# Kernel tuning notes

Hardware: AMD Instinct MI355X
Metric: run time of the kernel (lower is better)

## Reference

```python
import jax, jax.numpy as jnp
import numpy as np

HEADS = 8
MODEL_DIM = 64
IN_DIM = 512
FF_DIM = 2048
LN_EPS = 1e-5


def _ln(t, g, b):
    m = t.mean(-1, keepdims=True)
    v = ((t - m) ** 2).mean(-1, keepdims=True)
    return (t - m) * jax.lax.rsqrt(v + LN_EPS) * g + b


def setup_inputs() -> dict:
    key = jax.random.key(0)
    ks = jax.random.split(key, 12)
    s = 1.0 / np.sqrt(IN_DIM)
    x = jax.random.normal(ks[0], (8, 32, 32, IN_DIM), dtype=jnp.float32)
    Wq = jax.random.uniform(ks[1], (IN_DIM, HEADS * MODEL_DIM), jnp.float32, -s, s)
    Wk = jax.random.uniform(ks[2], (IN_DIM, HEADS * MODEL_DIM), jnp.float32, -s, s)
    Wv = jax.random.uniform(ks[3], (IN_DIM, HEADS * MODEL_DIM), jnp.float32, -s, s)
    Wo = jax.random.uniform(ks[4], (HEADS * MODEL_DIM, IN_DIM), jnp.float32, -s, s)
    ln1_g = jnp.ones((IN_DIM,), jnp.float32)
    ln1_b = jnp.zeros((IN_DIM,), jnp.float32)
    fc1_w = jax.random.uniform(ks[5], (IN_DIM, FF_DIM), jnp.float32, -s, s)
    fc1_b = jnp.zeros((FF_DIM,), jnp.float32)
    s2 = 1.0 / np.sqrt(FF_DIM)
    fc2_w = jax.random.uniform(ks[6], (FF_DIM, IN_DIM), jnp.float32, -s2, s2)
    fc2_b = jnp.zeros((IN_DIM,), jnp.float32)
    ln2_g = jnp.ones((IN_DIM,), jnp.float32)
    ln2_b = jnp.zeros((IN_DIM,), jnp.float32)
    return {"x": x, "Wq": Wq, "Wk": Wk, "Wv": Wv, "Wo": Wo,
            "ln1_g": ln1_g, "ln1_b": ln1_b,
            "fc1_w": fc1_w, "fc1_b": fc1_b, "fc2_w": fc2_w, "fc2_b": fc2_b,
            "ln2_g": ln2_g, "ln2_b": ln2_b}


def reference(x, Wq, Wk, Wv, Wo, ln1_g, ln1_b, fc1_w, fc1_b, fc2_w, fc2_b, ln2_g, ln2_b):
    bs, h, w, c = x.shape
    # --- BertSelfAttention (pre_norm=True) ---
    xn = _ln(x, ln1_g, ln1_b)
    Q = (xn @ Wq).reshape(bs, h, w, HEADS, MODEL_DIM)
    K = (xn @ Wk).reshape(bs, h, w, HEADS, MODEL_DIM)
    V = (xn @ Wv).reshape(bs, h, w, HEADS, MODEL_DIM)
    scores = jnp.einsum('bijhd,bklhd->bijhkl', Q, K) / jnp.sqrt(jnp.float32(MODEL_DIM))
    probs = jax.nn.softmax(scores.reshape(bs, h, w, HEADS, h * w), axis=-1)
    probs = probs.reshape(bs, h, w, HEADS, h, w)
    o = jnp.einsum('bijhkl,bklhd->bijhd', probs, V).reshape(bs, h, w, HEADS * MODEL_DIM)
    attn_out = o @ Wo + xn  # residual adds pre-normed x (as in the torch code)
    # --- Feedforward (pre_norm=True) ---
    yn = _ln(attn_out, ln2_g, ln2_b)
    out = jax.nn.relu(yn @ fc1_w + fc1_b) @ fc2_w + fc2_b + yn
    return (out, probs)
```

## Files before the change

### kernel.cpp

```cpp
#include <hip/hip_runtime.h>

typedef unsigned short u16;
typedef unsigned int   u32;
typedef short s16x8 __attribute__((ext_vector_type(8)));
typedef float f32x4 __attribute__((ext_vector_type(4)));

#define EPI_QK  0
#define EPI_VT  1
#define EPI_RES 2
#define EPI_FC1 3
#define EPI_FC2 4

__device__ __forceinline__ u16 f2bf(float f) {
    u32 u = __float_as_uint(f);
    u32 r = u + 0x7FFFu + ((u >> 16) & 1u);
    return (u16)(r >> 16);
}
__device__ __forceinline__ s16x8 ld8(const u16* p) {
    return *(const s16x8*)p;
}
__device__ __forceinline__ void gload_lds16(const void* g, void* l) {
    __builtin_amdgcn_global_load_lds(
        (const __attribute__((address_space(1))) unsigned int*)g,
        (__attribute__((address_space(3))) unsigned int*)l, 16, 0, 0);
}


__device__ __forceinline__ void transpose_body(
    const float* __restrict__ W, u16* __restrict__ Wt, int Kd, int Nd,
    int bx, int by, float (*tls)[33])
{
    const int k0 = bx * 32, n0 = by * 32;
    const int r = threadIdx.x >> 3, c4 = (threadIdx.x & 7) * 4;
    float4 v = *(const float4*)&W[(size_t)(k0 + r) * Nd + n0 + c4];
    tls[r][c4] = v.x; tls[r][c4 + 1] = v.y; tls[r][c4 + 2] = v.z; tls[r][c4 + 3] = v.w;
    __syncthreads();
    u32 lo = (u32)f2bf(tls[c4][r])     | ((u32)f2bf(tls[c4 + 1][r]) << 16);
    u32 hi = (u32)f2bf(tls[c4 + 2][r]) | ((u32)f2bf(tls[c4 + 3][r]) << 16);
    uint2 pk; pk.x = lo; pk.y = hi;
    *(uint2*)&Wt[(size_t)(n0 + r) * Kd + k0 + c4] = pk;
}

__device__ __forceinline__ void ln_body(
    const float* __restrict__ x, const float* __restrict__ g, const float* __restrict__ bb,
    float* __restrict__ of, u16* __restrict__ ob, int tb)
{
    const int wave = threadIdx.x >> 6, lane = threadIdx.x & 63;
    const int t = tb * 4 + wave;
    const float* row = x + (size_t)t * 512;
    float4 v0 = *(const float4*)&row[lane * 8];
    float4 v1 = *(const float4*)&row[lane * 8 + 4];
    float s  = v0.x + v0.y + v0.z + v0.w + v1.x + v1.y + v1.z + v1.w;
    float sq = v0.x*v0.x + v0.y*v0.y + v0.z*v0.z + v0.w*v0.w
             + v1.x*v1.x + v1.y*v1.y + v1.z*v1.z + v1.w*v1.w;
#pragma unroll
    for (int o = 1; o < 64; o <<= 1) { s += __shfl_xor(s, o, 64); sq += __shfl_xor(sq, o, 64); }
    float mean = s * (1.f / 512.f);
    float var  = sq * (1.f / 512.f) - mean * mean;
    float rs = rsqrtf(var + 1e-5f);
    float4 g0 = *(const float4*)&g[lane * 8];
    float4 g1 = *(const float4*)&g[lane * 8 + 4];
    float4 b0 = *(const float4*)&bb[lane * 8];
    float4 b1 = *(const float4*)&bb[lane * 8 + 4];
    float y[8];
    y[0] = (v0.x - mean) * rs * g0.x + b0.x;
    y[1] = (v0.y - mean) * rs * g0.y + b0.y;
    y[2] = (v0.z - mean) * rs * g0.z + b0.z;
    y[3] = (v0.w - mean) * rs * g0.w + b0.w;
    y[4] = (v1.x - mean) * rs * g1.x + b1.x;
    y[5] = (v1.y - mean) * rs * g1.y + b1.y;
    y[6] = (v1.z - mean) * rs * g1.z + b1.z;
    y[7] = (v1.w - mean) * rs * g1.w + b1.w;
    float4 o0; o0.x = y[0]; o0.y = y[1]; o0.z = y[2]; o0.w = y[3];
    float4 o1; o1.x = y[4]; o1.y = y[5]; o1.z = y[6]; o1.w = y[7];
    *(float4*)&of[(size_t)t * 512 + lane * 8]     = o0;
    *(float4*)&of[(size_t)t * 512 + lane * 8 + 4] = o1;
    uint4 pb;
    pb.x = (u32)f2bf(y[0]) | ((u32)f2bf(y[1]) << 16);
    pb.y = (u32)f2bf(y[2]) | ((u32)f2bf(y[3]) << 16);
    pb.z = (u32)f2bf(y[4]) | ((u32)f2bf(y[5]) << 16);
    pb.w = (u32)f2bf(y[6]) | ((u32)f2bf(y[7]) << 16);
    *(uint4*)&ob[(size_t)t * 512 + lane * 8] = pb;
}

__device__ __forceinline__ void gemm_loop(
    const u16* __restrict__ A, const u16* __restrict__ Bt,
    int K, int m0, int n0, u16* sA, u16* sB, f32x4 (&acc)[4][4])
{
    const int tid = threadIdx.x;
    const int wave = tid >> 6, lane = tid & 63;
    const int wr = (wave >> 1) * 64, wc = (wave & 1) * 64;
    const int lr = lane & 15, quad = lane >> 4;

    const int p0 = wave * 64 + lane;
    const int r0 = p0 >> 2,          c0 = p0 & 3;
    const int r1 = (p0 + 256) >> 2;
    const u16* gA0 = A  + (size_t)(m0 + r0) * K + c0 * 8;
    const u16* gA1 = A  + (size_t)(m0 + r1) * K + c0 * 8;
    const u16* gB0 = Bt + (size_t)(n0 + r0) * K + c0 * 8;
    const u16* gB1 = Bt + (size_t)(n0 + r1) * K + c0 * 8;
    u16* lA0 = sA + (size_t)(wave * 64) * 8;
    u16* lA1 = sA + (size_t)(256 + wave * 64) * 8;
    u16* lB0 = sB + (size_t)(wave * 64) * 8;
    u16* lB1 = sB + (size_t)(256 + wave * 64) * 8;

    for (int k0 = 0; k0 < K; k0 += 32) {
        __syncthreads();
        gload_lds16(gA0 + k0, lA0);
        gload_lds16(gA1 + k0, lA1);
        gload_lds16(gB0 + k0, lB0);
        gload_lds16(gB1 + k0, lB1);
        __syncthreads();
        s16x8 a[4], b[4];
#pragma unroll
        for (int i = 0; i < 4; i++) a[i] = ld8(&sA[(wr + i * 16 + lr) * 32 + quad * 8]);
#pragma unroll
        for (int j = 0; j < 4; j++) b[j] = ld8(&sB[(wc + j * 16 + lr) * 32 + quad * 8]);
#pragma unroll
        for (int i = 0; i < 4; i++)
#pragma unroll
            for (int j = 0; j < 4; j++)
                acc[i][j] = __builtin_amdgcn_mfma_f32_16x16x32_bf16(a[i], b[j], acc[i][j], 0, 0, 0);
    }
}

__global__ __launch_bounds__(256) void prep_kernel(
    const float* __restrict__ Wq, const float* __restrict__ Wk,
    const float* __restrict__ Wv, const float* __restrict__ Wo,
    const float* __restrict__ fc1_w, const float* __restrict__ fc2_w,
    u16* __restrict__ WqT, u16* __restrict__ WkT, u16* __restrict__ WvT,
    u16* __restrict__ WoT, u16* __restrict__ fc1T, u16* __restrict__ fc2T,
    const float* __restrict__ x, const float* __restrict__ g,
    const float* __restrict__ bb, float* __restrict__ of, u16* __restrict__ ob)
{
    __shared__ float tls[32][33];
    const int id = blockIdx.x;
    if (id < 1024) {
        const int sel = id >> 8, r = id & 255;
        const float* W = (sel == 0) ? Wq : (sel == 1) ? Wk : (sel == 2) ? Wv : Wo;
        u16* Wt        = (sel == 0) ? WqT : (sel == 1) ? WkT : (sel == 2) ? WvT : WoT;
        transpose_body(W, Wt, 512, 512, r & 15, r >> 4, tls);
    } else if (id < 2048) {
        const int r = id - 1024;
        transpose_body(fc1_w, fc1T, 512, 2048, r & 15, r >> 4, tls);
    } else if (id < 3072) {
        const int r = id - 2048;
        transpose_body(fc2_w, fc2T, 2048, 512, r & 63, r >> 6, tls);
    } else {
        ln_body(x, g, bb, of, ob, id - 3072);
    }
}

__global__ __launch_bounds__(256) void ln_kernel(
    const float* __restrict__ x, const float* __restrict__ g, const float* __restrict__ bb,
    float* __restrict__ of, u16* __restrict__ ob)
{
    ln_body(x, g, bb, of, ob, blockIdx.x);
}

__global__ __launch_bounds__(256) void qkvt_gemm(
    const u16* __restrict__ xn_b, const u16* __restrict__ WqT, const u16* __restrict__ WvT,
    u16* __restrict__ Q_s, u16* __restrict__ K_s, u16* __restrict__ Vt_s)
{
    __shared__ u16 sA[128 * 32];
    __shared__ u16 sB[128 * 32];
    const int id = blockIdx.x;
    const u16 *A, *Bt;
    int m0, n0, epi;
    if (id < 512) { epi = EPI_QK; A = xn_b; Bt = WqT; n0 = (id & 7) * 128;  m0 = (id >> 3) * 128; }
    else { const int i2 = id - 512;
           epi = EPI_VT; A = WvT;  Bt = xn_b; n0 = (i2 & 63) * 128; m0 = (i2 >> 6) * 128; }

    f32x4 acc[4][4] = {};
    gemm_loop(A, Bt, 512, m0, n0, sA, sB, acc);

    const int lane = threadIdx.x & 63, wave = threadIdx.x >> 6;
    const int wr = (wave >> 1) * 64, wc = (wave & 1) * 64;
    const int lr = lane & 15, quad = lane >> 4;
#pragma unroll
    for (int i = 0; i < 4; i++)
#pragma unroll
    for (int j = 0; j < 4; j++)
#pragma unroll
    for (int r = 0; r < 4; r++) {
        int row = m0 + wr + i * 16 + quad * 4 + r;
        int col = n0 + wc + j * 16 + lr;
        float v = acc[i][j][r];
        if (epi == EPI_QK) {
            u16* dst = (col < 512) ? Q_s : K_s;
            int c2 = col & 511;
            size_t idx = (size_t)((row >> 10) * 8 + (c2 >> 6)) * 65536
                       + (size_t)(row & 1023) * 64 + (c2 & 63);
            dst[idx] = f2bf(v);
        } else {
            size_t idx = (size_t)((col >> 10) * 8 + (row >> 6)) * 65536
                       + (size_t)(row & 63) * 1024 + (col & 1023);
            Vt_s[idx] = f2bf(v);
        }
    }
}

template<int EPI>
__global__ __launch_bounds__(256) void gemm128(
    const u16* __restrict__ A, const u16* __restrict__ Bt,
    void* __restrict__ Out, void* __restrict__ Out2,
    const float* __restrict__ bias, const float* __restrict__ res,
    int M, int N, int K)
{
    __shared__ u16 sA[128 * 32];
    __shared__ u16 sB[128 * 32];
    const int n0 = blockIdx.x * 128, m0 = blockIdx.y * 128;

    f32x4 acc[4][4] = {};
    gemm_loop(A, Bt, K, m0, n0, sA, sB, acc);

    const int lane = threadIdx.x & 63, wave = threadIdx.x >> 6;
    const int wr = (wave >> 1) * 64, wc = (wave & 1) * 64;
    const int lr = lane & 15, quad = lane >> 4;
#pragma unroll
    for (int i = 0; i < 4; i++)
#pragma unroll
    for (int j = 0; j < 4; j++)
#pragma unroll
    for (int r = 0; r < 4; r++) {
        int row = m0 + wr + i * 16 + quad * 4 + r;
        int col = n0 + wc + j * 16 + lr;
        float v = acc[i][j][r];
        if (EPI == EPI_RES) {
            size_t idx = (size_t)row * N + col;
            ((float*)Out)[idx] = v + res[idx];
        } else if (EPI == EPI_FC1) {
            v += bias[col];
            v = fmaxf(v, 0.f);
            ((u16*)Out)[(size_t)row * N + col] = f2bf(v);
        } else {
            size_t idx = (size_t)row * N + col;
            ((float*)Out)[idx] = v + bias[col] + res[idx];
        }
    }
}

__global__ __launch_bounds__(256) void attn_kernel(
    const u16* __restrict__ Qs, const u16* __restrict__ Ks, const u16* __restrict__ Vts,
    float* __restrict__ probs, u16* __restrict__ Os)
{
    __shared__ u16 sK[2][64 * 72];
    __shared__ u16 sV[2][64 * 72];
    __shared__ u16 sP[4][16 * 72];
    const int bh = blockIdx.x;
    const int q0 = blockIdx.y * 64;
    const int b = bh >> 3, h = bh & 7;
    const int tid = threadIdx.x, wave = tid >> 6, lane = tid & 63;
    const int lr = lane & 15, quad = lane >> 4;
    const float scale = 0.125f;

    const u16* qb = Qs + (size_t)bh * 65536 + (size_t)(q0 + wave * 16 + lr) * 64 + quad * 8;
    const s16x8 bq0 = ld8(qb);
    const s16x8 bq1 = ld8(qb + 32);

    const int sr0 = tid >> 3, sr1 = sr0 + 32;
    const int sc  = (tid & 7) * 8;
    const u16* Kg = Ks  + (size_t)bh * 65536;
    const u16* Vg = Vts + (size_t)bh * 65536;

    {
        uint4 a0 = *(const uint4*)&Kg[(size_t)sr0 * 64 + sc];
        uint4 a1 = *(const uint4*)&Kg[(size_t)sr1 * 64 + sc];
        *(uint4*)&sK[0][sr0 * 72 + sc] = a0;
        *(uint4*)&sK[0][sr1 * 72 + sc] = a1;
    }
    float lsum = 0.f;
    int cur = 0;
    for (int kt = 0; kt < 16; ++kt) {
        __syncthreads();
        uint4 pk0, pk1;
        const bool pf = (kt + 1 < 16);
        if (pf) {
            const u16* kn = Kg + (size_t)(kt + 1) * 4096;
            pk0 = *(const uint4*)&kn[(size_t)sr0 * 64 + sc];
            pk1 = *(const uint4*)&kn[(size_t)sr1 * 64 + sc];
        }
        f32x4 s[4] = {};
#pragma unroll
        for (int ks = 0; ks < 2; ++ks) {
            const s16x8 bq = ks ? bq1 : bq0;
#pragma unroll
            for (int j = 0; j < 4; j++) {
                s16x8 ak = ld8(&sK[cur][(j * 16 + lr) * 72 + ks * 32 + quad * 8]);
                s[j] = __builtin_amdgcn_mfma_f32_16x16x32_bf16(ak, bq, s[j], 0, 0, 0);
            }
        }
#pragma unroll
        for (int j = 0; j < 4; j++)
#pragma unroll
            for (int r = 0; r < 4; r++) lsum += __expf(s[j][r] * scale);
        if (pf) {
            *(uint4*)&sK[cur ^ 1][sr0 * 72 + sc] = pk0;
            *(uint4*)&sK[cur ^ 1][sr1 * 72 + sc] = pk1;
        }
        cur ^= 1;
    }
    lsum += __shfl_xor(lsum, 16, 64);
    lsum += __shfl_xor(lsum, 32, 64);
    const float linv = 1.f / lsum;

    {
        uint4 a0 = *(const uint4*)&Kg[(size_t)sr0 * 64 + sc];
        uint4 a1 = *(const uint4*)&Kg[(size_t)sr1 * 64 + sc];
        uint4 b0 = *(const uint4*)&Vg[(size_t)sr0 * 1024 + sc];
        uint4 b1 = *(const uint4*)&Vg[(size_t)sr1 * 1024 + sc];
        *(uint4*)&sK[0][sr0 * 72 + sc] = a0;
        *(uint4*)&sK[0][sr1 * 72 + sc] = a1;
        *(uint4*)&sV[0][sr0 * 72 + sc] = b0;
        *(uint4*)&sV[0][sr1 * 72 + sc] = b1;
    }
    float* pbase = probs + ((size_t)(b * 1024 + q0 + wave * 16 + lr)) * 8192
                 + h * 1024 + quad * 4;
    f32x4 o[4] = {};
    cur = 0;
    for (int kt = 0; kt < 16; ++kt) {
        __syncthreads();
        uint4 pk0, pk1, pv0, pv1;
        const bool pf = (kt + 1 < 16);
        if (pf) {
            const u16* kn = Kg + (size_t)(kt + 1) * 4096;
            const u16* vn = Vg + (size_t)(kt + 1) * 64;
            pk0 = *(const uint4*)&kn[(size_t)sr0 * 64 + sc];
            pk1 = *(const uint4*)&kn[(size_t)sr1 * 64 + sc];
            pv0 = *(const uint4*)&vn[(size_t)sr0 * 1024 + sc];
            pv1 = *(const uint4*)&vn[(size_t)sr1 * 1024 + sc];
        }
        f32x4 s[4] = {};
#pragma unroll
        for (int ks = 0; ks < 2; ++ks) {
            const s16x8 bq = ks ? bq1 : bq0;
#pragma unroll
            for (int j = 0; j < 4; j++) {
                s16x8 ak = ld8(&sK[cur][(j * 16 + lr) * 72 + ks * 32 + quad * 8]);
                s[j] = __builtin_amdgcn_mfma_f32_16x16x32_bf16(ak, bq, s[j], 0, 0, 0);
            }
        }
#pragma unroll
        for (int j = 0; j < 4; j++) {
            float p0 = __expf(s[j][0] * scale) * linv;
            float p1 = __expf(s[j][1] * scale) * linv;
            float p2 = __expf(s[j][2] * scale) * linv;
            float p3 = __expf(s[j][3] * scale) * linv;
            f32x4 pq; pq[0] = p0; pq[1] = p1; pq[2] = p2; pq[3] = p3;
            __builtin_nontemporal_store(pq, (f32x4*)&pbase[kt * 64 + j * 16]);
            uint2 pb2;
            pb2.x = (u32)f2bf(p0) | ((u32)f2bf(p1) << 16);
            pb2.y = (u32)f2bf(p2) | ((u32)f2bf(p3) << 16);
            *(uint2*)&sP[wave][lr * 72 + j * 16 + quad * 4] = pb2;
        }
        asm volatile("s_waitcnt lgkmcnt(0)" ::: "memory");
#pragma unroll
        for (int ks = 0; ks < 2; ++ks) {
            s16x8 a = ld8(&sP[wave][lr * 72 + ks * 32 + quad * 8]);
#pragma unroll
            for (int jd = 0; jd < 4; jd++) {
                s16x8 bv = ld8(&sV[cur][(jd * 16 + lr) * 72 + ks * 32 + quad * 8]);
                o[jd] = __builtin_amdgcn_mfma_f32_16x16x32_bf16(a, bv, o[jd], 0, 0, 0);
            }
        }
        if (pf) {
            *(uint4*)&sK[cur ^ 1][sr0 * 72 + sc] = pk0;
            *(uint4*)&sK[cur ^ 1][sr1 * 72 + sc] = pk1;
            *(uint4*)&sV[cur ^ 1][sr0 * 72 + sc] = pv0;
            *(uint4*)&sV[cur ^ 1][sr1 * 72 + sc] = pv1;
        }
        cur ^= 1;
    }
#pragma unroll
    for (int jd = 0; jd < 4; jd++)
#pragma unroll
    for (int r = 0; r < 4; r++) {
        int q = q0 + wave * 16 + quad * 4 + r;
        int d = jd * 16 + lr;
        Os[(size_t)(b * 1024 + q) * 512 + h * 64 + d] = f2bf(o[jd][r]);
    }
}

extern "C" void kernel_launch(void* const* d_in, const int* in_sizes, int n_in,
                              void* d_out, int out_size, void* d_ws, size_t ws_size,
                              hipStream_t stream)
{
    const float* x     = (const float*)d_in[0];
    const float* Wq    = (const float*)d_in[1];
    const float* Wk    = (const float*)d_in[2];
    const float* Wv    = (const float*)d_in[3];
    const float* Wo    = (const float*)d_in[4];
    const float* ln1_g = (const float*)d_in[5];
    const float* ln1_b = (const float*)d_in[6];
    const float* fc1_w = (const float*)d_in[7];
    const float* fc1_b = (const float*)d_in[8];
    const float* fc2_w = (const float*)d_in[9];
    const float* fc2_b = (const float*)d_in[10];
    const float* ln2_g = (const float*)d_in[11];
    const float* ln2_b = (const float*)d_in[12];

    char* ws = (char*)d_ws;
    const size_t MB = 1024 * 1024;
    u16*   Q_s    = (u16*)(ws + 0);
    u16*   K_s    = (u16*)(ws + 8 * MB);
    u16*   Vt_s   = (u16*)(ws + 16 * MB);
    u16*   O_s    = (u16*)(ws + 24 * MB);
    u16*   hidden = (u16*)(ws + 0);
    float* xn_f   = (float*)(ws + 32 * MB);
    u16*   xn_b   = (u16*)(ws + 48 * MB);
    float* aout   = (float*)(ws + 56 * MB);
    float* yn_f   = (float*)(ws + 72 * MB);
    u16*   yn_b   = (u16*)(ws + 88 * MB);
    u16*   WqT  = (u16*)(ws + 96 * MB);
    u16*   WkT  = WqT + 512 * 512;
    u16*   WvT  = WkT + 512 * 512;
    u16*   WoT  = WvT + 512 * 512;
    u16*   fc1T = WoT + 512 * 512;
    u16*   fc2T = fc1T + 2048 * 512;

    float* out0  = (float*)d_out;
    float* probs = out0 + 4194304;

    dim3 blk(256);

    prep_kernel<<<5120, blk, 0, stream>>>(
        Wq, Wk, Wv, Wo, fc1_w, fc2_w,
        WqT, WkT, WvT, WoT, fc1T, fc2T,
        x, ln1_g, ln1_b, xn_f, xn_b);

    qkvt_gemm<<<768, blk, 0, stream>>>(xn_b, WqT, WvT, Q_s, K_s, Vt_s);

    attn_kernel<<<dim3(64, 16), blk, 0, stream>>>(Q_s, K_s, Vt_s, probs, O_s);

    gemm128<EPI_RES><<<dim3(4, 64), blk, 0, stream>>>(
        O_s, WoT, aout, nullptr, nullptr, xn_f, 8192, 512, 512);

    ln_kernel<<<2048, blk, 0, stream>>>(aout, ln2_g, ln2_b, yn_f, yn_b);

    gemm128<EPI_FC1><<<dim3(16, 64), blk, 0, stream>>>(
        yn_b, fc1T, hidden, nullptr, fc1_b, nullptr, 8192, 2048, 512);
    gemm128<EPI_FC2><<<dim3(4, 64), blk, 0, stream>>>(
        hidden, fc2T, out0, nullptr, fc2_b, yn_f, 8192, 512, 2048);
}
```

Baseline: 525.6 us.

## Cache unnormalized exp scores in registers; use 64-row GEMM tiles for N=512

The attention kernel now stores bf16-packed exponentials from the first pass in registers (16x4 uint2 per thread). The second pass reuses them instead of reloading K and recomputing QK^T and exp, and normalization moves to the output with a shuffled per-row inverse sum. This removes half the QK MFMAs and the second K stream, at the cost of much higher register pressure from the fully unrolled loops. Probabilities written to the output are now derived from bf16-rounded exponentials, which lowers their precision. Separately, a new gemm64 kernel with 64x128 tiles doubles the block count for the two N=512 GEMMs to improve occupancy across CUs.

```diff
diff --git a/kernel.cpp b/kernel.cpp
--- a/kernel.cpp
+++ b/kernel.cpp
@@ -240,6 +240,68 @@
     }
 }
 
+template<int EPI>
+__global__ __launch_bounds__(256) void gemm64(
+    const u16* __restrict__ A, const u16* __restrict__ Bt,
+    void* __restrict__ Out,
+    const float* __restrict__ bias, const float* __restrict__ res,
+    int M, int N, int K)
+{
+    __shared__ u16 sA[64 * 32];
+    __shared__ u16 sB[128 * 32];
+    const int tid = threadIdx.x;
+    const int wave = tid >> 6, lane = tid & 63;
+    const int n0 = blockIdx.x * 128, m0 = blockIdx.y * 64;
+    const int wr = (wave >> 1) * 32, wc = (wave & 1) * 64;
+    const int lr = lane & 15, quad = lane >> 4;
+
+    const int p0 = wave * 64 + lane;
+    const int ra = p0 >> 2, c0 = p0 & 3;
+    const int rb1 = (p0 + 256) >> 2;
+    const u16* gA0 = A  + (size_t)(m0 + ra) * K + c0 * 8;
+    const u16* gB0 = Bt + (size_t)(n0 + ra) * K + c0 * 8;
+    const u16* gB1 = Bt + (size_t)(n0 + rb1) * K + c0 * 8;
+    u16* lA0 = sA + (size_t)(wave * 64) * 8;
+    u16* lB0 = sB + (size_t)(wave * 64) * 8;
+    u16* lB1 = sB + (size_t)(256 + wave * 64) * 8;
+
+    f32x4 acc[2][4] = {};
+    for (int k0 = 0; k0 < K; k0 += 32) {
+        __syncthreads();
+        gload_lds16(gA0 + k0, lA0);
+        gload_lds16(gB0 + k0, lB0);
+        gload_lds16(gB1 + k0, lB1);
+        __syncthreads();
+        s16x8 a[2], bfr[4];
+#pragma unroll
+        for (int i = 0; i < 2; i++) a[i] = ld8(&sA[(wr + i * 16 + lr) * 32 + quad * 8]);
+#pragma unroll
+        for (int j = 0; j < 4; j++) bfr[j] = ld8(&sB[(wc + j * 16 + lr) * 32 + quad * 8]);
+#pragma unroll
+        for (int i = 0; i < 2; i++)
+#pragma unroll
+            for (int j = 0; j < 4; j++)
+                acc[i][j] = __builtin_amdgcn_mfma_f32_16x16x32_bf16(a[i], bfr[j], acc[i][j], 0, 0, 0);
+    }
+
+#pragma unroll
+    for (int i = 0; i < 2; i++)
+#pragma unroll
+    for (int j = 0; j < 4; j++)
+#pragma unroll
+    for (int r = 0; r < 4; r++) {
+        int row = m0 + wr + i * 16 + quad * 4 + r;
+        int col = n0 + wc + j * 16 + lr;
+        float v = acc[i][j][r];
+        size_t idx = (size_t)row * N + col;
+        if (EPI == EPI_RES) {
+            ((float*)Out)[idx] = v + res[idx];
+        } else {
+            ((float*)Out)[idx] = v + bias[col] + res[idx];
+        }
+    }
+}
+
 __global__ __launch_bounds__(256) void attn_kernel(
     const u16* __restrict__ Qs, const u16* __restrict__ Ks, const u16* __restrict__ Vts,
     float* __restrict__ probs, u16* __restrict__ Os)
@@ -263,14 +325,17 @@
     const u16* Kg = Ks  + (size_t)bh * 65536;
     const u16* Vg = Vts + (size_t)bh * 65536;
 
+    uint2 pe[16][4];
+    float lsum = 0.f;
+
     {
         uint4 a0 = *(const uint4*)&Kg[(size_t)sr0 * 64 + sc];
         uint4 a1 = *(const uint4*)&Kg[(size_t)sr1 * 64 + sc];
         *(uint4*)&sK[0][sr0 * 72 + sc] = a0;
         *(uint4*)&sK[0][sr1 * 72 + sc] = a1;
     }
-    float lsum = 0.f;
     int cur = 0;
+#pragma unroll
     for (int kt = 0; kt < 16; ++kt) {
         __syncthreads();
         uint4 pk0, pk1;
@@ -291,9 +356,15 @@
             }
         }
 #pragma unroll
-        for (int j = 0; j < 4; j++)
-#pragma unroll
-            for (int r = 0; r < 4; r++) lsum += __expf(s[j][r] * scale);
+        for (int j = 0; j < 4; j++) {
+            float e0 = __expf(s[j][0] * scale);
+            float e1 = __expf(s[j][1] * scale);
+            float e2 = __expf(s[j][2] * scale);
+            float e3 = __expf(s[j][3] * scale);
+            lsum += (e0 + e1) + (e2 + e3);
+            pe[kt][j].x = (u32)f2bf(e0) | ((u32)f2bf(e1) << 16);
+            pe[kt][j].y = (u32)f2bf(e2) | ((u32)f2bf(e3) << 16);
+        }
         if (pf) {
             *(uint4*)&sK[cur ^ 1][sr0 * 72 + sc] = pk0;
             *(uint4*)&sK[cur ^ 1][sr1 * 72 + sc] = pk1;
@@ -303,14 +374,13 @@
     lsum += __shfl_xor(lsum, 16, 64);
     lsum += __shfl_xor(lsum, 32, 64);
     const float linv = 1.f / lsum;
+    float l4[4];
+#pragma unroll
+    for (int r = 0; r < 4; r++) l4[r] = __shfl(linv, quad * 4 + r, 64);
 
     {
-        uint4 a0 = *(const uint4*)&Kg[(size_t)sr0 * 64 + sc];
-        uint4 a1 = *(const uint4*)&Kg[(size_t)sr1 * 64 + sc];
         uint4 b0 = *(const uint4*)&Vg[(size_t)sr0 * 1024 + sc];
         uint4 b1 = *(const uint4*)&Vg[(size_t)sr1 * 1024 + sc];
-        *(uint4*)&sK[0][sr0 * 72 + sc] = a0;
-        *(uint4*)&sK[0][sr1 * 72 + sc] = a1;
         *(uint4*)&sV[0][sr0 * 72 + sc] = b0;
         *(uint4*)&sV[0][sr1 * 72 + sc] = b1;
     }
@@ -318,40 +388,26 @@
                  + h * 1024 + quad * 4;
     f32x4 o[4] = {};
     cur = 0;
+#pragma unroll
     for (int kt = 0; kt < 16; ++kt) {
         __syncthreads();
-        uint4 pk0, pk1, pv0, pv1;
+        uint4 pv0, pv1;
         const bool pf = (kt + 1 < 16);
         if (pf) {
-            const u16* kn = Kg + (size_t)(kt + 1) * 4096;
             const u16* vn = Vg + (size_t)(kt + 1) * 64;
-            pk0 = *(const uint4*)&kn[(size_t)sr0 * 64 + sc];
-            pk1 = *(const uint4*)&kn[(size_t)sr1 * 64 + sc];
             pv0 = *(const uint4*)&vn[(size_t)sr0 * 1024 + sc];
             pv1 = *(const uint4*)&vn[(size_t)sr1 * 1024 + sc];
         }
-        f32x4 s[4] = {};
-#pragma unroll
-        for (int ks = 0; ks < 2; ++ks) {
-            const s16x8 bq = ks ? bq1 : bq0;
-#pragma unroll
-            for (int j = 0; j < 4; j++) {
-                s16x8 ak = ld8(&sK[cur][(j * 16 + lr) * 72 + ks * 32 + quad * 8]);
-                s[j] = __builtin_amdgcn_mfma_f32_16x16x32_bf16(ak, bq, s[j], 0, 0, 0);
-            }
-        }
 #pragma unroll
         for (int j = 0; j < 4; j++) {
-            float p0 = __expf(s[j][0] * scale) * linv;
-            float p1 = __expf(s[j][1] * scale) * linv;
-            float p2 = __expf(s[j][2] * scale) * linv;
-            float p3 = __expf(s[j][3] * scale) * linv;
-            f32x4 pq; pq[0] = p0; pq[1] = p1; pq[2] = p2; pq[3] = p3;
+            const uint2 pk = pe[kt][j];
+            float e0 = __uint_as_float(pk.x << 16);
+            float e1 = __uint_as_float(pk.x & 0xffff0000u);
+            float e2 = __uint_as_float(pk.y << 16);
+            float e3 = __uint_as_float(pk.y & 0xffff0000u);
+            f32x4 pq; pq[0] = e0 * linv; pq[1] = e1 * linv; pq[2] = e2 * linv; pq[3] = e3 * linv;
             __builtin_nontemporal_store(pq, (f32x4*)&pbase[kt * 64 + j * 16]);
-            uint2 pb2;
-            pb2.x = (u32)f2bf(p0) | ((u32)f2bf(p1) << 16);
-            pb2.y = (u32)f2bf(p2) | ((u32)f2bf(p3) << 16);
-            *(uint2*)&sP[wave][lr * 72 + j * 16 + quad * 4] = pb2;
+            *(uint2*)&sP[wave][lr * 72 + j * 16 + quad * 4] = pk;
         }
         asm volatile("s_waitcnt lgkmcnt(0)" ::: "memory");
 #pragma unroll
@@ -364,8 +420,6 @@
             }
         }
         if (pf) {
-            *(uint4*)&sK[cur ^ 1][sr0 * 72 + sc] = pk0;
-            *(uint4*)&sK[cur ^ 1][sr1 * 72 + sc] = pk1;
             *(uint4*)&sV[cur ^ 1][sr0 * 72 + sc] = pv0;
             *(uint4*)&sV[cur ^ 1][sr1 * 72 + sc] = pv1;
         }
@@ -377,7 +431,7 @@
     for (int r = 0; r < 4; r++) {
         int q = q0 + wave * 16 + quad * 4 + r;
         int d = jd * 16 + lr;
-        Os[(size_t)(b * 1024 + q) * 512 + h * 64 + d] = f2bf(o[jd][r]);
+        Os[(size_t)(b * 1024 + q) * 512 + h * 64 + d] = f2bf(o[jd][r] * l4[r]);
     }
 }
 
@@ -432,13 +486,13 @@
 
     attn_kernel<<<dim3(64, 16), blk, 0, stream>>>(Q_s, K_s, Vt_s, probs, O_s);
 
-    gemm128<EPI_RES><<<dim3(4, 64), blk, 0, stream>>>(
-        O_s, WoT, aout, nullptr, nullptr, xn_f, 8192, 512, 512);
+    gemm64<EPI_RES><<<dim3(4, 128), blk, 0, stream>>>(
+        O_s, WoT, aout, nullptr, xn_f, 8192, 512, 512);
 
     ln_kernel<<<2048, blk, 0, stream>>>(aout, ln2_g, ln2_b, yn_f, yn_b);
 
     gemm128<EPI_FC1><<<dim3(16, 64), blk, 0, stream>>>(
         yn_b, fc1T, hidden, nullptr, fc1_b, nullptr, 8192, 2048, 512);
-    gemm128<EPI_FC2><<<dim3(4, 64), blk, 0, stream>>>(
-        hidden, fc2T, out0, nullptr, fc2_b, yn_f, 8192, 512, 2048);
-}
+    gemm64<EPI_FC2><<<dim3(4, 128), blk, 0, stream>>>(
+        hidden, fc2T, out0, fc2_b, yn_f, 8192, 512, 2048);
+}
```

Measured after the change: 506.6 us. 1.04x faster.
